# Kernel optimization log

Measured on AMD Instinct MI355X. Metric: run time of the kernel, lower is better.

## Reference

```python
import jax, jax.numpy as jnp
import numpy as np

C = 5  # number of part/class tokens (hard-coded in the torch module)


def _parts(N):
    h = (N - C) // 2
    q = (N - C) // 4
    tq = (N - C) * 3 // 4
    # token ranges per part, matching `partlist` / the if/elif slicing
    return [(C, N), (C, N), (C, C + h), (C + q, C + tq), (C + h, N)]


def setup_inputs() -> dict:
    key = jax.random.key(0)
    k1, k2 = jax.random.split(key)
    L, b, N, D = 12, 64, 201, 768
    x = jax.random.normal(k1, (L, b, N, N), dtype=jnp.float32)
    features = jax.random.normal(k2, (b, N, D), dtype=jnp.float32)
    return {"x": x, "features": features}


def reference(x, features):
    # x: [L, b, N, N] stacked per-layer attention maps; features: [b, N, D]
    L, b, N, _ = x.shape
    cams = []
    for e, (s, t) in enumerate(_parts(N)):
        # gather row/col e plus the part's token range -> [L, b, 1+P, 1+P]
        idx = jnp.concatenate([jnp.array([e], dtype=jnp.int32),
                               jnp.arange(s, t, dtype=jnp.int32)])
        sub = x[:, :, idx][:, :, :, idx]
        # attention rollout: att[L-1] @ ... @ att[1] @ att[0]
        last = sub[0]
        for i in range(1, L):
            last = jnp.matmul(sub[i], last)
        w = last[:, 0:1, 1:]                      # [b, 1, P]
        fm = jax.nn.relu(features[:, s:t])        # [b, P, D]
        cams.append(jnp.matmul(w, fm))            # [b, 1, D]
    feat_cam = jnp.concatenate(cams, axis=1)      # [b, C, D]
    return feat_cam[:, 1:]                        # [b, C-1, D]
```

## Files before the change

kernel.cpp:

```cpp
#include <hip/hip_runtime.h>


#define L_ 12
#define B_ 64
#define N_ 201
#define D_ 768
#define NN_ ((size_t)N_ * N_)

#define RING 6
#define LEAD 5

#define BAR() asm volatile("s_waitcnt lgkmcnt(0)\n\ts_barrier" ::: "memory")
#define WAITC(n) asm volatile("s_waitcnt vmcnt(" #n ")" ::: "memory")

__device__ __forceinline__ void glds4(const float* g, float* l) {
    __builtin_amdgcn_global_load_lds(
        (const __attribute__((address_space(1))) void*)g,
        (__attribute__((address_space(3))) void*)l, 4, 0, 0);
}

template<int RP, int NQ>
__device__ __forceinline__ float* run_chain(
    const float* __restrict__ x, int b, int e, int s, int M,
    float* vin, float* vout, float* ring, float* vpart, float* partial,
    int tid)
{
    const int lane = tid & 63;
    const int wr   = tid >> 6;
    const int QT   = NQ * 64;

    int cadd[4];
    #pragma unroll
    for (int i = 0; i < NQ; ++i) {
        int q  = i * 64 + lane;
        int qc = (q < M) ? q : (M - 1);
        cadd[i] = (q == 0) ? e : (s - 1 + qc);
    }

    auto ISSUE = [&](const float* xl, int ji, int isl) {
        int rr = wr * RP + ji;
        int rc = (rr < M) ? rr : (M - 1);
        int ra = (rc == 0) ? e : (s + rc - 1);
        const float* rowp = xl + (size_t)ra * N_;
        float* sb = ring + (size_t)(wr * RING + isl) * 256;
        #pragma unroll
        for (int i = 0; i < NQ; ++i)
            glds4(rowp + cadd[i], sb + i * 64);
    };

    const float* xli = x + ((size_t)10 * B_ + b) * NN_;
    #pragma unroll
    for (int g = 0; g < LEAD; ++g) ISSUE(xli, g, g);
    int ji = LEAD;
    int sl = 0;

    BAR();

    float a0 = 0.f, a1 = 0.f, a2 = 0.f, a3 = 0.f;

    auto CONSUME = [&](int j) {
        const float* sb = ring + (size_t)(wr * RING + sl) * 256;
        float vj = vin[wr * RP + j];
        if (NQ == 4) {
            float4 mv = *(const float4*)(sb + lane * 4);
            a0 += vj * mv.x; a1 += vj * mv.y; a2 += vj * mv.z; a3 += vj * mv.w;
        } else {
            float2 mv = *(const float2*)(sb + lane * 2);
            a0 += vj * mv.x; a1 += vj * mv.y;
        }
    };

    auto REDUCE = [&]() {
        if (NQ == 4)
            *(float4*)&vpart[(wr << 8) + (lane << 2)] = make_float4(a0, a1, a2, a3);
        else
            *(float2*)&vpart[wr * 128 + lane * 2] = make_float2(a0, a1);
        BAR();
        if (NQ == 4) {
            int tg = tid >> 8, q = tid & 255;
            partial[tg * 256 + q] =
                vpart[(tg * 4 + 0) * 256 + q] + vpart[(tg * 4 + 1) * 256 + q] +
                vpart[(tg * 4 + 2) * 256 + q] + vpart[(tg * 4 + 3) * 256 + q];
        } else {
            int tg = tid >> 7, q = tid & 127;
            partial[tg * 128 + q] =
                vpart[(tg * 2 + 0) * 128 + q] + vpart[(tg * 2 + 1) * 128 + q];
        }
        BAR();
        if (tid < QT) {
            float v = 0.f;
            if (NQ == 4) {
                v = partial[tid] + partial[256 + tid] + partial[512 + tid] + partial[768 + tid];
            } else {
                #pragma unroll
                for (int g = 0; g < 8; ++g) v += partial[g * 128 + tid];
            }
            vout[tid] = (tid < M) ? v : 0.f;
        }
        BAR();
        float* t = vin; vin = vout; vout = t;
        a0 = a1 = a2 = a3 = 0.f;
    };

    for (int l = 10; l >= 1; --l) {
        #pragma unroll
        for (int j = 0; j < RP; ++j) {
            if (NQ == 4) { WAITC(16); } else { WAITC(8); }
            CONSUME(j);
            {
                int isl = sl + LEAD; if (isl >= RING) isl -= RING;
                ISSUE(xli, ji, isl);
            }
            ji++;
            if (ji == RP) { ji = 0; xli -= (size_t)B_ * NN_; }
            sl = (sl + 1 == RING) ? 0 : sl + 1;
        }
        REDUCE();
    }

    #pragma unroll
    for (int j = 0; j < RP; ++j) {
        if (j < RP - LEAD) {
            if (NQ == 4) { WAITC(16); } else { WAITC(8); }
        } else if (j == RP - LEAD) {
            WAITC(0);
        }
        CONSUME(j);
        if (j < RP - LEAD) {
            int isl = sl + LEAD; if (isl >= RING) isl -= RING;
            ISSUE(xli, ji, isl);
            ji++;
        }
        sl = (sl + 1 == RING) ? 0 : sl + 1;
    }
    REDUCE();
    return vin;
}

__global__ __launch_bounds__(1024) void part_cam_chain(
    const float* __restrict__ x,
    const float* __restrict__ feat,
    float* __restrict__ out,
    float* __restrict__ wbuf)
{
    __shared__ __align__(16) float ring[16 * RING * 256];
    __shared__ __align__(16) float vpart[16 * 256];
    __shared__ __align__(16) float partial[1024];
    __shared__ __align__(16) float bufA[256];
    __shared__ __align__(16) float bufB[256];

    const int p = blockIdx.x >> 6;
    const int b = blockIdx.x & 63;
    const int e = p + 1;
    const int s = (p == 0) ? 5 : (p == 1) ? 5 : (p == 2) ? 54 : 103;
    const int t = (p == 0) ? 201 : (p == 1) ? 103 : (p == 2) ? 152 : 201;
    const int K = t - s;
    const int M = K + 1;
    const int tid = threadIdx.x;

    if (tid < 256) { bufA[tid] = 0.f; bufB[tid] = 0.f; }
    if (tid < M) {
        const float* m11 = x + ((size_t)11 * B_ + b) * NN_;
        bufA[tid] = m11[(size_t)e * N_ + ((tid == 0) ? e : (s + tid - 1))];
    }

    float* vf = (p == 0)
        ? run_chain<13, 4>(x, b, e, s, M, bufA, bufB, ring, vpart, partial, tid)
        : run_chain<7, 2>(x, b, e, s, M, bufA, bufB, ring, vpart, partial, tid);

    if (p == 0) {
        if (tid < 256) wbuf[b * 256 + tid] = (tid >= 1 && tid <= K) ? vf[tid] : 0.f;
    } else {
        if (tid < D_) {
            const float* fb = feat + (size_t)b * N_ * D_ + tid;
            float acc = 0.f;
            for (int k = 0; k < 98; k += 8) {
                float f[8];
                #pragma unroll
                for (int jj = 0; jj < 8; ++jj)
                    if (k + jj < K) f[jj] = fb[(size_t)(s + k + jj) * D_];
                #pragma unroll
                for (int jj = 0; jj < 8; ++jj)
                    if (k + jj < K) acc += vf[1 + k + jj] * fmaxf(f[jj], 0.f);
            }
            out[((size_t)b * 4 + p) * D_ + tid] = acc;
        }
    }
}

__global__ __launch_bounds__(256) void part_cam_epi0(
    const float* __restrict__ feat,
    const float* __restrict__ wbuf,
    float* __restrict__ out)
{
    const int b  = blockIdx.x / 3;
    const int dc = blockIdx.x % 3;
    const int tid = threadIdx.x;
    __shared__ float wsh[256];
    wsh[tid] = wbuf[b * 256 + tid];
    __syncthreads();
    const int d = dc * 256 + tid;
    const float* fb = feat + (size_t)b * N_ * D_ + d;
    float acc = 0.f;
    for (int k = 0; k < 196; k += 16) {
        float f[16];
        #pragma unroll
        for (int jj = 0; jj < 16; ++jj)
            if (k + jj < 196) f[jj] = fb[(size_t)(5 + k + jj) * D_];
        #pragma unroll
        for (int jj = 0; jj < 16; ++jj)
            if (k + jj < 196) acc += wsh[1 + k + jj] * fmaxf(f[jj], 0.f);
    }
    out[((size_t)b * 4 + 0) * D_ + d] = acc;
}

extern "C" void kernel_launch(void* const* d_in, const int* in_sizes, int n_in,
                              void* d_out, int out_size, void* d_ws, size_t ws_size,
                              hipStream_t stream) {
    const float* x    = (const float*)d_in[0];
    const float* feat = (const float*)d_in[1];
    float* out = (float*)d_out;
    float* w   = (float*)d_ws;
    part_cam_chain<<<dim3(256), dim3(1024), 0, stream>>>(x, feat, out, w);
    part_cam_epi0<<<dim3(192), dim3(256), 0, stream>>>(feat, w, out);
}
```

Before: 87.64 us.

## Merge the four part chains into one masked chain per batch

Each batch's four part rollouts previously ran in separate blocks on gathered submatrices. They now run in one block that streams full 201x201 rows once and updates four masked vectors together, using in_part masks to stand in for the gathers. All four part epilogues move to a separate, wider epilogue kernel. The aim is to cut redundant global loads. The cost is a quarter as many blocks and four serialized reduce/barrier passes per layer, which lengthens the critical path.

```diff
diff --git a/kernel.cpp b/kernel.cpp
--- a/kernel.cpp
+++ b/kernel.cpp
@@ -7,8 +7,9 @@
 #define D_ 768
 #define NN_ ((size_t)N_ * N_)
 
-#define RING 6
-#define LEAD 5
+#define RING 8
+#define LEAD 6
+#define RP 13
 
 #define BAR() asm volatile("s_waitcnt lgkmcnt(0)\n\ts_barrier" ::: "memory")
 #define WAITC(n) asm volatile("s_waitcnt vmcnt(" #n ")" ::: "memory")
@@ -19,112 +20,115 @@
         (__attribute__((address_space(3))) void*)l, 4, 0, 0);
 }
 
-template<int RP, int NQ>
-__device__ __forceinline__ float* run_chain(
-    const float* __restrict__ x, int b, int e, int s, int M,
-    float* vin, float* vout, float* ring, float* vpart, float* partial,
-    int tid)
+__device__ __forceinline__ bool in_part(int p, int g) {
+    const int e = p + 1;
+    const int s = (p == 0) ? 5 : (p == 1) ? 5 : (p == 2) ? 54 : 103;
+    const int t = (p == 0) ? 201 : (p == 1) ? 103 : (p == 2) ? 152 : 201;
+    return (g == e) || (g >= s && g < t);
+}
+
+__global__ __launch_bounds__(1024) void part_cam_chain(
+    const float* __restrict__ x,
+    float* __restrict__ wbuf)
 {
+    __shared__ __align__(16) float ring[16 * RING * 256];
+    __shared__ __align__(16) float vAll[256 * 4];
+    __shared__ __align__(16) float red[16 * 256];
+
+    const int b    = blockIdx.x;
+    const int tid  = threadIdx.x;
     const int lane = tid & 63;
-    const int wr   = tid >> 6;
-    const int QT   = NQ * 64;
+    const int w    = tid >> 6;
 
     int cadd[4];
     #pragma unroll
-    for (int i = 0; i < NQ; ++i) {
-        int q  = i * 64 + lane;
-        int qc = (q < M) ? q : (M - 1);
-        cadd[i] = (q == 0) ? e : (s - 1 + qc);
+    for (int i = 0; i < 4; ++i) {
+        int col = i * 64 + lane;
+        cadd[i] = (col <= 200) ? col : 200;
     }
 
-    auto ISSUE = [&](const float* xl, int ji, int isl) {
-        int rr = wr * RP + ji;
-        int rc = (rr < M) ? rr : (M - 1);
-        int ra = (rc == 0) ? e : (s + rc - 1);
-        const float* rowp = xl + (size_t)ra * N_;
-        float* sb = ring + (size_t)(wr * RING + isl) * 256;
+    auto ISSUE = [&](const float* xl, int j, int isl) {
+        int rr = 1 + w * RP + j;
+        if (rr > 200) rr = 0;
+        const float* rowp = xl + (size_t)rr * N_;
+        float* sb = ring + (((size_t)w * RING + isl) << 8);
         #pragma unroll
-        for (int i = 0; i < NQ; ++i)
+        for (int i = 0; i < 4; ++i)
             glds4(rowp + cadd[i], sb + i * 64);
     };
 
+    float iv0 = 0.f, iv1 = 0.f, iv2 = 0.f, iv3 = 0.f;
+    if (tid < 256) {
+        const float* x11 = x + ((size_t)11 * B_ + b) * NN_;
+        const int g = (tid <= 200) ? tid : 200;
+        iv0 = x11[(size_t)1 * N_ + g];
+        iv1 = x11[(size_t)2 * N_ + g];
+        iv2 = x11[(size_t)3 * N_ + g];
+        iv3 = x11[(size_t)4 * N_ + g];
+    }
+
     const float* xli = x + ((size_t)10 * B_ + b) * NN_;
     #pragma unroll
-    for (int g = 0; g < LEAD; ++g) ISSUE(xli, g, g);
-    int ji = LEAD;
-    int sl = 0;
+    for (int g0 = 0; g0 < LEAD; ++g0) ISSUE(xli, g0, g0);
+    int ji = LEAD, sl = 0;
 
+    if (tid < 256) {
+        vAll[tid * 4 + 0] = in_part(0, tid) ? iv0 : 0.f;
+        vAll[tid * 4 + 1] = in_part(1, tid) ? iv1 : 0.f;
+        vAll[tid * 4 + 2] = in_part(2, tid) ? iv2 : 0.f;
+        vAll[tid * 4 + 3] = in_part(3, tid) ? iv3 : 0.f;
+    }
     BAR();
 
-    float a0 = 0.f, a1 = 0.f, a2 = 0.f, a3 = 0.f;
+    float4 acc0 = {0,0,0,0}, acc1 = {0,0,0,0}, acc2 = {0,0,0,0}, acc3 = {0,0,0,0};
 
     auto CONSUME = [&](int j) {
-        const float* sb = ring + (size_t)(wr * RING + sl) * 256;
-        float vj = vin[wr * RP + j];
-        if (NQ == 4) {
-            float4 mv = *(const float4*)(sb + lane * 4);
-            a0 += vj * mv.x; a1 += vj * mv.y; a2 += vj * mv.z; a3 += vj * mv.w;
-        } else {
-            float2 mv = *(const float2*)(sb + lane * 2);
-            a0 += vj * mv.x; a1 += vj * mv.y;
-        }
+        const float* sb = ring + (((size_t)w * RING + sl) << 8);
+        float4 xv = *(const float4*)(sb + lane * 4);
+        int rr = 1 + w * RP + j;
+        if (rr > 200) rr = 0;
+        float4 vv = *(const float4*)(vAll + rr * 4);
+        acc0.x += vv.x * xv.x; acc0.y += vv.x * xv.y; acc0.z += vv.x * xv.z; acc0.w += vv.x * xv.w;
+        acc1.x += vv.y * xv.x; acc1.y += vv.y * xv.y; acc1.z += vv.y * xv.z; acc1.w += vv.y * xv.w;
+        acc2.x += vv.z * xv.x; acc2.y += vv.z * xv.y; acc2.z += vv.z * xv.z; acc2.w += vv.z * xv.w;
+        acc3.x += vv.w * xv.x; acc3.y += vv.w * xv.y; acc3.z += vv.w * xv.z; acc3.w += vv.w * xv.w;
     };
 
     auto REDUCE = [&]() {
-        if (NQ == 4)
-            *(float4*)&vpart[(wr << 8) + (lane << 2)] = make_float4(a0, a1, a2, a3);
-        else
-            *(float2*)&vpart[wr * 128 + lane * 2] = make_float2(a0, a1);
-        BAR();
-        if (NQ == 4) {
-            int tg = tid >> 8, q = tid & 255;
-            partial[tg * 256 + q] =
-                vpart[(tg * 4 + 0) * 256 + q] + vpart[(tg * 4 + 1) * 256 + q] +
-                vpart[(tg * 4 + 2) * 256 + q] + vpart[(tg * 4 + 3) * 256 + q];
-        } else {
-            int tg = tid >> 7, q = tid & 127;
-            partial[tg * 128 + q] =
-                vpart[(tg * 2 + 0) * 128 + q] + vpart[(tg * 2 + 1) * 128 + q];
+        #pragma unroll
+        for (int pp = 0; pp < 4; ++pp) {
+            float4 a = (pp == 0) ? acc0 : (pp == 1) ? acc1 : (pp == 2) ? acc2 : acc3;
+            *(float4*)&red[(w << 8) + (lane << 2)] = a;
+            BAR();
+            if (tid < 256) {
+                float sum = 0.f;
+                #pragma unroll
+                for (int ww = 0; ww < 16; ++ww) sum += red[(ww << 8) + tid];
+                vAll[tid * 4 + pp] = in_part(pp, tid) ? sum : 0.f;
+            }
+            BAR();
         }
-        BAR();
-        if (tid < QT) {
-            float v = 0.f;
-            if (NQ == 4) {
-                v = partial[tid] + partial[256 + tid] + partial[512 + tid] + partial[768 + tid];
-            } else {
-                #pragma unroll
-                for (int g = 0; g < 8; ++g) v += partial[g * 128 + tid];
-            }
-            vout[tid] = (tid < M) ? v : 0.f;
-        }
-        BAR();
-        float* t = vin; vin = vout; vout = t;
-        a0 = a1 = a2 = a3 = 0.f;
+        acc0 = make_float4(0,0,0,0); acc1 = make_float4(0,0,0,0);
+        acc2 = make_float4(0,0,0,0); acc3 = make_float4(0,0,0,0);
     };
 
     for (int l = 10; l >= 1; --l) {
         #pragma unroll
         for (int j = 0; j < RP; ++j) {
-            if (NQ == 4) { WAITC(16); } else { WAITC(8); }
+            WAITC(20);
             CONSUME(j);
-            {
-                int isl = sl + LEAD; if (isl >= RING) isl -= RING;
-                ISSUE(xli, ji, isl);
-            }
+            int isl = sl + LEAD; if (isl >= RING) isl -= RING;
+            ISSUE(xli, ji, isl);
             ji++;
             if (ji == RP) { ji = 0; xli -= (size_t)B_ * NN_; }
             sl = (sl + 1 == RING) ? 0 : sl + 1;
         }
         REDUCE();
     }
-
     #pragma unroll
     for (int j = 0; j < RP; ++j) {
-        if (j < RP - LEAD) {
-            if (NQ == 4) { WAITC(16); } else { WAITC(8); }
-        } else if (j == RP - LEAD) {
-            WAITC(0);
-        }
+        if (j < RP - LEAD) { WAITC(20); }
+        else if (j == RP - LEAD) { WAITC(0); }
         CONSUME(j);
         if (j < RP - LEAD) {
             int isl = sl + LEAD; if (isl >= RING) isl -= RING;
@@ -134,84 +138,47 @@
         sl = (sl + 1 == RING) ? 0 : sl + 1;
     }
     REDUCE();
-    return vin;
-}
 
-__global__ __launch_bounds__(1024) void part_cam_chain(
-    const float* __restrict__ x,
-    const float* __restrict__ feat,
-    float* __restrict__ out,
-    float* __restrict__ wbuf)
-{
-    __shared__ __align__(16) float ring[16 * RING * 256];
-    __shared__ __align__(16) float vpart[16 * 256];
-    __shared__ __align__(16) float partial[1024];
-    __shared__ __align__(16) float bufA[256];
-    __shared__ __align__(16) float bufB[256];
-
-    const int p = blockIdx.x >> 6;
-    const int b = blockIdx.x & 63;
-    const int e = p + 1;
-    const int s = (p == 0) ? 5 : (p == 1) ? 5 : (p == 2) ? 54 : 103;
-    const int t = (p == 0) ? 201 : (p == 1) ? 103 : (p == 2) ? 152 : 201;
-    const int K = t - s;
-    const int M = K + 1;
-    const int tid = threadIdx.x;
-
-    if (tid < 256) { bufA[tid] = 0.f; bufB[tid] = 0.f; }
-    if (tid < M) {
-        const float* m11 = x + ((size_t)11 * B_ + b) * NN_;
-        bufA[tid] = m11[(size_t)e * N_ + ((tid == 0) ? e : (s + tid - 1))];
-    }
-
-    float* vf = (p == 0)
-        ? run_chain<13, 4>(x, b, e, s, M, bufA, bufB, ring, vpart, partial, tid)
-        : run_chain<7, 2>(x, b, e, s, M, bufA, bufB, ring, vpart, partial, tid);
-
-    if (p == 0) {
-        if (tid < 256) wbuf[b * 256 + tid] = (tid >= 1 && tid <= K) ? vf[tid] : 0.f;
-    } else {
-        if (tid < D_) {
-            const float* fb = feat + (size_t)b * N_ * D_ + tid;
-            float acc = 0.f;
-            for (int k = 0; k < 98; k += 8) {
-                float f[8];
-                #pragma unroll
-                for (int jj = 0; jj < 8; ++jj)
-                    if (k + jj < K) f[jj] = fb[(size_t)(s + k + jj) * D_];
-                #pragma unroll
-                for (int jj = 0; jj < 8; ++jj)
-                    if (k + jj < K) acc += vf[1 + k + jj] * fmaxf(f[jj], 0.f);
-            }
-            out[((size_t)b * 4 + p) * D_ + tid] = acc;
-        }
+    {
+        int p = tid >> 8, k = tid & 255;
+        const int sp = (p == 0) ? 5 : (p == 1) ? 5 : (p == 2) ? 54 : 103;
+        const int Kp = (p == 0) ? 196 : 98;
+        float val = (k < Kp) ? vAll[(sp + k) * 4 + p] : 0.f;
+        wbuf[((size_t)p * B_ + b) * 256 + k] = val;
     }
 }
 
-__global__ __launch_bounds__(256) void part_cam_epi0(
+__global__ __launch_bounds__(256) void part_cam_epi(
     const float* __restrict__ feat,
     const float* __restrict__ wbuf,
     float* __restrict__ out)
 {
-    const int b  = blockIdx.x / 3;
-    const int dc = blockIdx.x % 3;
+    const int bid = blockIdx.x;
+    const int b   = bid / 12;
+    const int rem = bid % 12;
+    const int p   = rem / 3;
+    const int dc  = rem % 3;
+    const int s = (p == 0) ? 5 : (p == 1) ? 5 : (p == 2) ? 54 : 103;
+    const int K = (p == 0) ? 196 : 98;
     const int tid = threadIdx.x;
+
     __shared__ float wsh[256];
-    wsh[tid] = wbuf[b * 256 + tid];
+    wsh[tid] = wbuf[((size_t)p * B_ + b) * 256 + tid];
     __syncthreads();
+
     const int d = dc * 256 + tid;
     const float* fb = feat + (size_t)b * N_ * D_ + d;
     float acc = 0.f;
-    for (int k = 0; k < 196; k += 16) {
+    for (int k = 0; k < K; k += 16) {
         float f[16];
         #pragma unroll
         for (int jj = 0; jj < 16; ++jj)
-            if (k + jj < 196) f[jj] = fb[(size_t)(5 + k + jj) * D_];
+            if (k + jj < K) f[jj] = fb[(size_t)(s + k + jj) * D_];
         #pragma unroll
         for (int jj = 0; jj < 16; ++jj)
-            if (k + jj < 196) acc += wsh[1 + k + jj] * fmaxf(f[jj], 0.f);
+            if (k + jj < K) acc += wsh[k + jj] * fmaxf(f[jj], 0.f);
     }
-    out[((size_t)b * 4 + 0) * D_ + d] = acc;
+    out[((size_t)b * 4 + p) * D_ + d] = acc;
 }
 
 extern "C" void kernel_launch(void* const* d_in, const int* in_sizes, int n_in,
@@ -221,6 +188,6 @@
     const float* feat = (const float*)d_in[1];
     float* out = (float*)d_out;
     float* w   = (float*)d_ws;
-    part_cam_chain<<<dim3(256), dim3(1024), 0, stream>>>(x, feat, out, w);
-    part_cam_epi0<<<dim3(192), dim3(256), 0, stream>>>(feat, w, out);
+    part_cam_chain<<<dim3(64), dim3(1024), 0, stream>>>(x, w);
+    part_cam_epi<<<dim3(768), dim3(256), 0, stream>>>(feat, w, out);
 }
```

New measurement: 131.9 us. 1.51x slower.
